# Optimization experiments

Hardware: AMD Instinct MI355X
Metric: run time of the kernel (lower is better)

## Reference

```python
import jax, jax.numpy as jnp
import numpy as np

B, S, HID = 1, 2048, 4096
NH, NKV, D = 32, 8, 128          # query heads, kv heads, head_dim
GROUPS = NH // NKV               # GQA repeat factor = 4
WINDOW = 1024                    # sliding-window size
ROPE_BASE = 10000.0


def setup_inputs() -> dict:
    key = jax.random.key(0)
    k = jax.random.split(key, 5)
    hidden_states = jax.random.normal(k[0], (B, S, HID), jnp.float32)
    Wq = jax.random.normal(k[1], (HID, HID), jnp.float32) * 0.02
    Wk = jax.random.normal(k[2], (NKV * D, HID), jnp.float32) * 0.02
    Wv = jax.random.normal(k[3], (NKV * D, HID), jnp.float32) * 0.02
    Wo = jax.random.normal(k[4], (HID, HID), jnp.float32) * 0.02
    position_ids = jnp.arange(S, dtype=jnp.int64 if jax.config.jax_enable_x64 else jnp.int32)[None, :]
    # Sliding-window causal additive mask [B,1,S,S]: key j visible to query i iff i-WINDOW < j <= i
    i = jnp.arange(S)
    visible = (i[None, :] <= i[:, None]) & (i[:, None] - i[None, :] < WINDOW)
    neg = jnp.finfo(jnp.float32).min
    attention_mask = jnp.where(visible, 0.0, neg)[None, None, :, :].astype(jnp.float32)
    return {"hidden_states": hidden_states, "attention_mask": attention_mask,
            "position_ids": position_ids, "Wq": Wq, "Wk": Wk, "Wv": Wv, "Wo": Wo}


def _rotate_half(x):
    x1, x2 = x[..., : D // 2], x[..., D // 2:]
    return jnp.concatenate((-x2, x1), axis=-1)


def _rope_cos_sin(position_ids, dtype):
    # inv_freq over even dims; gather-by-position_ids == direct indexing
    inv_freq = 1.0 / (ROPE_BASE ** (jnp.arange(0, D, 2, dtype=jnp.float32) / D))  # [D/2]
    freqs = position_ids.astype(jnp.float32)[..., None] * inv_freq                # [B,S,D/2]
    emb = jnp.concatenate((freqs, freqs), axis=-1)                                # [B,S,D]
    cos = jnp.cos(emb)[:, None, :, :].astype(dtype)                               # [B,1,S,D]
    sin = jnp.sin(emb)[:, None, :, :].astype(dtype)
    return cos, sin


def reference(hidden_states, attention_mask, position_ids, Wq, Wk, Wv, Wo):
    bsz, q_len, _ = hidden_states.shape
    # projections (nn.Linear: y = x @ W.T)
    q = (hidden_states @ Wq.T).reshape(bsz, q_len, NH, D).transpose(0, 2, 1, 3)    # [B,NH,S,D]
    k = (hidden_states @ Wk.T).reshape(bsz, q_len, NKV, D).transpose(0, 2, 1, 3)   # [B,NKV,S,D]
    v = (hidden_states @ Wv.T).reshape(bsz, q_len, NKV, D).transpose(0, 2, 1, 3)
    cos, sin = _rope_cos_sin(position_ids, q.dtype)
    q = q * cos + _rotate_half(q) * sin
    k = k * cos + _rotate_half(k) * sin
    # GQA repeat_kv (repeat_interleave along head dim)
    k = jnp.repeat(k, GROUPS, axis=1)                                              # [B,NH,S,D]
    v = jnp.repeat(v, GROUPS, axis=1)
    scores = jnp.einsum('bhqd,bhkd->bhqk', q, k) / np.sqrt(D)                       # [B,NH,S,S]
    scores = scores + attention_mask
    scores = jnp.maximum(scores, jnp.finfo(scores.dtype).min)
    probs = jax.nn.softmax(scores.astype(jnp.float32), axis=-1).astype(q.dtype)
    out = jnp.einsum('bhqk,bhkd->bhqd', probs, v)                                   # [B,NH,S,D]
    out = out.transpose(0, 2, 1, 3).reshape(bsz, q_len, HID)
    return out @ Wo.T
```

## Files before the change

### kernel.cpp

```cpp
#include <hip/hip_runtime.h>

#define S_LEN 2048
#define HID   4096
#define NH    32
#define NKV   8
#define DH    128
#define KVD   (NKV*DH)
#define WIN   1024
#define NTOT  6144

typedef __bf16 bf16_t;
typedef __bf16 bfrag  __attribute__((ext_vector_type(8)));
typedef __bf16 bf4    __attribute__((ext_vector_type(4)));
typedef float  ffrag  __attribute__((ext_vector_type(4)));
typedef float  f4     __attribute__((ext_vector_type(4)));

__global__ __launch_bounds__(256) void f32_to_bf16_kernel(const float* __restrict__ src,
                                                          bf16_t* __restrict__ dst, int n4) {
  int i = blockIdx.x * 256 + threadIdx.x;
  if (i < n4) {
    ffrag v = *(const ffrag*)(src + (size_t)i * 4);
    bf4 o;
    o[0] = (bf16_t)v[0]; o[1] = (bf16_t)v[1]; o[2] = (bf16_t)v[2]; o[3] = (bf16_t)v[3];
    *(bf4*)(dst + (size_t)i * 4) = o;
  }
}

__global__ __launch_bounds__(256) void cvt4_kernel(const float* __restrict__ h,
    const float* __restrict__ Wq, const float* __restrict__ Wk, const float* __restrict__ Wv,
    bf16_t* __restrict__ hB, bf16_t* __restrict__ WqB,
    bf16_t* __restrict__ WkB, bf16_t* __restrict__ WvB) {
  int i = blockIdx.x * 256 + threadIdx.x;
  const int N0 = S_LEN * HID / 4;
  const int N1 = N0 + HID * HID / 4;
  const int N2 = N1 + KVD * HID / 4;
  const float* s; bf16_t* d; int off;
  if (i < N0)      { s = h;  d = hB;  off = i; }
  else if (i < N1) { s = Wq; d = WqB; off = i - N0; }
  else if (i < N2) { s = Wk; d = WkB; off = i - N1; }
  else             { s = Wv; d = WvB; off = i - N2; }
  ffrag v = *(const ffrag*)(s + (size_t)off * 4);
  bf4 o;
  o[0] = (bf16_t)v[0]; o[1] = (bf16_t)v[1]; o[2] = (bf16_t)v[2]; o[3] = (bf16_t)v[3];
  *(bf4*)(d + (size_t)off * 4) = o;
}


__device__ __forceinline__ void load_lds16(const bf16_t* g, bf16_t* l) {
  __builtin_amdgcn_global_load_lds((__attribute__((address_space(1))) void*)g,
                                   (__attribute__((address_space(3))) void*)l,
                                   16, 0, 0);
}

#define BARW() asm volatile("s_barrier" ::: "memory")
#define WAITV(n) asm volatile("s_waitcnt vmcnt(" #n ")" ::: "memory")
#define LGKM0() do { asm volatile("s_waitcnt lgkmcnt(0)" ::: "memory"); \
                     __builtin_amdgcn_sched_barrier(0); } while (0)

template <int OUT_MODE>
__device__ __forceinline__ void gemm_body(const bf16_t* __restrict__ A,
                                          const bf16_t* __restrict__ B,
                                          void* __restrict__ Cv,
                                          int row0, int col0,
                                          int N, bf16_t* lds) {
  constexpr int K     = 4096;
  constexpr int NT    = K / 64;
  constexpr int ABUFE = 256 * 64;
  constexpr int BBUFE = 64 * 64;

  bf16_t* As0 = lds;
  bf16_t* Bs0 = lds + 2 * ABUFE;

  const int tid  = threadIdx.x;
  const int wave = tid >> 6;
  const int lane = tid & 63;
  const int wr = wave >> 2, wc = wave & 3;
  const int n = lane & 15, qd = lane >> 4;

  const int rsub = tid >> 3;
  const int sg   = (tid & 7) ^ (rsub & 7);
  const bf16_t* Ag = A + (size_t)(row0 + rsub) * K + sg * 8;
  const bf16_t* Bg = B + (size_t)(col0 + rsub) * K + sg * 8;
  const int wbase = wave * 512;

  const int pg0 = ( qd      ^ (n & 7)) * 8;
  const int pg1 = ((4 | qd) ^ (n & 7)) * 8;
  const int abase = wr * 8192 + n * 64;
  const int bbase = wc * 1024 + n * 64;

  ffrag acc[8];
#pragma unroll
  for (int mt = 0; mt < 8; ++mt) {
    acc[mt][0] = 0.f; acc[mt][1] = 0.f; acc[mt][2] = 0.f; acc[mt][3] = 0.f;
  }

  auto STAGE = [&](int t, int s) {
    const int ko = t * 64;
    bf16_t* as = As0 + s * ABUFE + wbase;
#pragma unroll
    for (int i = 0; i < 4; ++i)
      load_lds16(Ag + (size_t)(i * 64) * K + ko, as + i * 4096);
    load_lds16(Bg + ko, Bs0 + s * BBUFE + wbase);
  };

  STAGE(0, 0); STAGE(1, 1);
  WAITV(5);
  BARW();

  for (int t = 0; t < NT; ++t) {
    const int s = t & 1;
    const bf16_t* Asl = As0 + s * ABUFE;
    const bf16_t* Bsl = Bs0 + s * BBUFE;
    bfrag av[8], bv;

#pragma unroll
    for (int mt = 0; mt < 8; ++mt) av[mt] = *(const bfrag*)(Asl + abase + mt * 1024 + pg0);
    bv = *(const bfrag*)(Bsl + bbase + pg0);
    __builtin_amdgcn_s_setprio(1);
#pragma unroll
    for (int mt = 0; mt < 8; ++mt)
      acc[mt] = __builtin_amdgcn_mfma_f32_16x16x32_bf16(av[mt], bv, acc[mt], 0, 0, 0);
    __builtin_amdgcn_s_setprio(0);

#pragma unroll
    for (int mt = 0; mt < 8; ++mt) av[mt] = *(const bfrag*)(Asl + abase + mt * 1024 + pg1);
    bv = *(const bfrag*)(Bsl + bbase + pg1);
    __builtin_amdgcn_s_setprio(1);
#pragma unroll
    for (int mt = 0; mt < 8; ++mt)
      acc[mt] = __builtin_amdgcn_mfma_f32_16x16x32_bf16(av[mt], bv, acc[mt], 0, 0, 0);
    __builtin_amdgcn_s_setprio(0);

    LGKM0();
    BARW();
    if (t + 2 < NT) STAGE(t + 2, s);
    if (t + 1 < NT) {
      if (t + 2 < NT) { WAITV(5); }
      else            { WAITV(0); }
      BARW();
    }
  }

  const int orow = row0 + wr * 128 + qd * 4;
  const int ocol = col0 + wc * 16 + n;
#pragma unroll
  for (int mt = 0; mt < 8; ++mt)
#pragma unroll
    for (int r = 0; r < 4; ++r) {
      size_t idx = (size_t)(orow + mt * 16 + r) * N + ocol;
      if (OUT_MODE == 1) ((bf16_t*)Cv)[idx] = (bf16_t)acc[mt][r];
      else               ((float*)Cv)[idx]  = acc[mt][r];
    }
}

__global__ __launch_bounds__(512, 4) void gemm_qkv_kernel(const bf16_t* __restrict__ hB,
                                                          const bf16_t* __restrict__ Wqkv,
                                                          bf16_t* __restrict__ C) {
  __shared__ __align__(16) bf16_t lds[2 * 256 * 64 + 2 * 64 * 64];
  const int raw  = blockIdx.x;
  const int xcd  = raw & 7;
  const int slot = raw >> 3;
  const int bx   = xcd * 12 + slot % 12;
  const int by   = slot / 12;
  gemm_body<1>(hB, Wqkv, C, by * 256, bx * 64, NTOT, lds);
}

__global__ __launch_bounds__(512, 4) void gemm_out_kernel(const bf16_t* __restrict__ A,
                                                          const bf16_t* __restrict__ B,
                                                          float* __restrict__ out) {
  __shared__ __align__(16) bf16_t lds[2 * 256 * 64 + 2 * 64 * 64];
  const int raw  = blockIdx.x;
  const int xcd  = raw & 7;
  const int slot = raw >> 3;
  const int bx   = xcd * 8 + (slot & 7);
  const int by   = slot >> 3;
  gemm_body<0>(A, B, out, by * 256, bx * 64, HID, lds);
}

__global__ __launch_bounds__(256) void ropecvt_kernel(const bf16_t* __restrict__ Cqkv,
                                                      bf16_t* __restrict__ Qb,
                                                      bf16_t* __restrict__ Kb,
                                                      bf16_t* __restrict__ Vb) {
  int idx = blockIdx.x * 256 + threadIdx.x;
  int g  = idx & 7;
  int t  = idx >> 3;
  int hh = t % 48;
  int s  = t / 48;
  const bf16_t* r0 = Cqkv + (size_t)s * NTOT + hh * 128;
  bfrag a0 = *(const bfrag*)&r0[g * 8];
  bfrag a1 = *(const bfrag*)&r0[g * 8 + 64];
  bf16_t* p;
  bool rope;
  if (hh < NH)           { p = Qb + (size_t)s * HID + hh * DH;        rope = true; }
  else if (hh < NH+NKV)  { p = Kb + (size_t)s * KVD + (hh - NH) * DH; rope = true; }
  else                   { p = Vb + (size_t)s * KVD + (hh - 40) * DH; rope = false; }
  bfrag o1, o2;
#pragma unroll
  for (int j = 0; j < 8; ++j) {
    float x1 = (float)a0[j];
    float x2 = (float)a1[j];
    if (rope) {
      int d = g * 8 + j;
      float inv = exp2f((float)d * (-13.287712379549449f / 64.f));
      float ang = (float)s * inv;
      float sn = sinf(ang), cs = cosf(ang);
      o1[j] = (bf16_t)(x1 * cs - x2 * sn);
      o2[j] = (bf16_t)(x2 * cs + x1 * sn);
    } else {
      o1[j] = (bf16_t)x1;
      o2[j] = (bf16_t)x2;
    }
  }
  *(bfrag*)&p[g * 8]      = o1;
  *(bfrag*)&p[g * 8 + 64] = o2;
}

#define KS_STRIDE 136
#define VT_STRIDE 72
#define PS_STRIDE 72

__global__ __launch_bounds__(256, 3) void attn_kernel(const bf16_t* __restrict__ Q,
                                                      const bf16_t* __restrict__ Kc,
                                                      const bf16_t* __restrict__ Vc,
                                                      bf16_t* __restrict__ AO) {
  const int qt   = 31 - blockIdx.x;
  const int h    = blockIdx.y;
  const int kvh  = h >> 2;
  const int q0   = qt * 64;
  const int tid  = threadIdx.x;
  const int wq   = tid >> 6;
  const int lane = tid & 63;
  const int n    = lane & 15;
  const int quad = lane >> 4;
  const float scale = 0.08838834764831845f;

  __shared__ __align__(16) bf16_t Ks[64 * KS_STRIDE];
  __shared__ __align__(16) bf16_t VT[128 * VT_STRIDE];
  __shared__ __align__(16) bf16_t Ps[4][16 * PS_STRIDE];

  bfrag aq[4];
#pragma unroll
  for (int kc = 0; kc < 4; ++kc) {
    bfrag t = *(const bfrag*)&Q[(size_t)(q0 + wq * 16 + n) * HID + h * DH + kc * 32 + quad * 8];
#pragma unroll
    for (int e = 0; e < 8; ++e) t[e] = (bf16_t)((float)t[e] * scale);
    aq[kc] = t;
  }

  ffrag acc[8];
#pragma unroll
  for (int dt = 0; dt < 8; ++dt) { acc[dt][0] = 0.f; acc[dt][1] = 0.f; acc[dt][2] = 0.f; acc[dt][3] = 0.f; }
  float lrow[4] = {0.f, 0.f, 0.f, 0.f};

  const int ktlo = (q0 >= WIN) ? ((q0 - (WIN - 1)) >> 6) : 0;
  const int kthi = (q0 + 63) >> 6;

  const int kg = tid & 15;
  const int dg = tid >> 4;

  bfrag pk[4], pv[4];
  {
    const int k0 = ktlo * 64;
#pragma unroll
    for (int i = 0; i < 4; ++i) {
      int pos = i * 256 + tid;
      pk[i] = *(const bfrag*)&Kc[(size_t)(k0 + (pos >> 4)) * KVD + kvh * DH + (pos & 15) * 8];
    }
#pragma unroll
    for (int j = 0; j < 4; ++j)
      pv[j] = *(const bfrag*)&Vc[(size_t)(k0 + j * 16 + kg) * KVD + kvh * DH + dg * 8];
  }

  for (int kt = ktlo; kt <= kthi; ++kt) {
    const int k0 = kt * 64;
    __syncthreads();
#pragma unroll
    for (int i = 0; i < 4; ++i) {
      int pos = i * 256 + tid;
      *(bfrag*)&Ks[(pos >> 4) * KS_STRIDE + (pos & 15) * 8] = pk[i];
    }
#pragma unroll
    for (int i = 0; i < 8; ++i) {
      bf4 pkk;
      pkk[0] = pv[0][i]; pkk[1] = pv[1][i]; pkk[2] = pv[2][i]; pkk[3] = pv[3][i];
      *(bf4*)&VT[(dg * 8 + i) * VT_STRIDE + kg * 4] = pkk;
    }
    __syncthreads();
    if (kt < kthi) {
      const int k1 = k0 + 64;
#pragma unroll
      for (int i = 0; i < 4; ++i) {
        int pos = i * 256 + tid;
        pk[i] = *(const bfrag*)&Kc[(size_t)(k1 + (pos >> 4)) * KVD + kvh * DH + (pos & 15) * 8];
      }
#pragma unroll
      for (int j = 0; j < 4; ++j)
        pv[j] = *(const bfrag*)&Vc[(size_t)(k1 + j * 16 + kg) * KVD + kvh * DH + dg * 8];
    }

    ffrag s[4];
#pragma unroll
    for (int nt = 0; nt < 4; ++nt) { s[nt][0] = 0.f; s[nt][1] = 0.f; s[nt][2] = 0.f; s[nt][3] = 0.f; }
#pragma unroll
    for (int kc = 0; kc < 4; ++kc) {
      bfrag bk[4];
#pragma unroll
      for (int nt = 0; nt < 4; ++nt)
        bk[nt] = *(const bfrag*)&Ks[(nt * 16 + n) * KS_STRIDE + kc * 32 + quad * 8];
      __builtin_amdgcn_s_setprio(1);
#pragma unroll
      for (int nt = 0; nt < 4; ++nt)
        s[nt] = __builtin_amdgcn_mfma_f32_16x16x32_bf16(aq[kc], bk[nt], s[nt], 0, 0, 0);
      __builtin_amdgcn_s_setprio(0);
    }

    const bool full = (k0 + 63 <= q0) && (q0 + 63 - k0 < WIN);
    if (!full) {
#pragma unroll
      for (int nt = 0; nt < 4; ++nt)
#pragma unroll
        for (int r = 0; r < 4; ++r) {
          int q = q0 + wq * 16 + quad * 4 + r;
          int k = k0 + nt * 16 + n;
          bool vis = (k <= q) && ((q - k) < WIN);
          if (!vis) s[nt][r] = -1e30f;
        }
    }

#pragma unroll
    for (int r = 0; r < 4; ++r) {
      bf4 pkk;
      float ps0 = __expf(s[0][r]);
      float ps1 = __expf(s[1][r]);
      float ps2 = __expf(s[2][r]);
      float ps3 = __expf(s[3][r]);
      lrow[r] += (ps0 + ps1) + (ps2 + ps3);
      pkk[0] = (bf16_t)ps0; pkk[1] = (bf16_t)ps1; pkk[2] = (bf16_t)ps2; pkk[3] = (bf16_t)ps3;
      *(bf4*)&Ps[wq][(quad * 4 + r) * PS_STRIDE + n * 4] = pkk;
    }

#pragma unroll
    for (int kc = 0; kc < 2; ++kc) {
      bfrag ap = *(const bfrag*)&Ps[wq][n * PS_STRIDE + kc * 32 + quad * 8];
#pragma unroll
      for (int dt = 0; dt < 8; dt += 4) {
        bfrag bv0 = *(const bfrag*)&VT[((dt + 0) * 16 + n) * VT_STRIDE + kc * 32 + quad * 8];
        bfrag bv1 = *(const bfrag*)&VT[((dt + 1) * 16 + n) * VT_STRIDE + kc * 32 + quad * 8];
        bfrag bv2 = *(const bfrag*)&VT[((dt + 2) * 16 + n) * VT_STRIDE + kc * 32 + quad * 8];
        bfrag bv3 = *(const bfrag*)&VT[((dt + 3) * 16 + n) * VT_STRIDE + kc * 32 + quad * 8];
        __builtin_amdgcn_s_setprio(1);
        acc[dt + 0] = __builtin_amdgcn_mfma_f32_16x16x32_bf16(ap, bv0, acc[dt + 0], 0, 0, 0);
        acc[dt + 1] = __builtin_amdgcn_mfma_f32_16x16x32_bf16(ap, bv1, acc[dt + 1], 0, 0, 0);
        acc[dt + 2] = __builtin_amdgcn_mfma_f32_16x16x32_bf16(ap, bv2, acc[dt + 2], 0, 0, 0);
        acc[dt + 3] = __builtin_amdgcn_mfma_f32_16x16x32_bf16(ap, bv3, acc[dt + 3], 0, 0, 0);
        __builtin_amdgcn_s_setprio(0);
      }
    }
  }

#pragma unroll
  for (int off = 1; off < 16; off <<= 1)
#pragma unroll
    for (int r = 0; r < 4; ++r) lrow[r] += __shfl_xor(lrow[r], off);
  float inv[4];
#pragma unroll
  for (int r = 0; r < 4; ++r) inv[r] = 1.f / lrow[r];
#pragma unroll
  for (int dt = 0; dt < 8; ++dt)
#pragma unroll
    for (int r = 0; r < 4; ++r)
      AO[(size_t)(q0 + wq * 16 + quad * 4 + r) * HID + h * DH + dt * 16 + n] =
          (bf16_t)(acc[dt][r] * inv[r]);
}

extern "C" void kernel_launch(void* const* d_in, const int* in_sizes, int n_in,
                              void* d_out, int out_size, void* d_ws, size_t ws_size,
                              hipStream_t stream) {
  const float* h  = (const float*)d_in[0];
  const float* Wq = (const float*)d_in[3];
  const float* Wk = (const float*)d_in[4];
  const float* Wv = (const float*)d_in[5];
  const float* Wo = (const float*)d_in[6];
  float* out = (float*)d_out;

  char* ws = (char*)d_ws;
  const size_t MB = (size_t)1 << 20;
  bf16_t* hB    = (bf16_t*)(ws + 0 * MB);
  bf16_t* Qb    = (bf16_t*)(ws + 0 * MB);
  bf16_t* WqB   = (bf16_t*)(ws + 16 * MB);
  bf16_t* WkB   = (bf16_t*)(ws + 48 * MB);
  bf16_t* WvB   = (bf16_t*)(ws + 56 * MB);
  bf16_t* Cqkv  = (bf16_t*)(ws + 64 * MB);
  bf16_t* WoB   = (bf16_t*)(ws + 64 * MB);
  bf16_t* AOb   = (bf16_t*)(ws + 96 * MB);
  bf16_t* Kb    = (bf16_t*)(ws + 112 * MB);
  bf16_t* Vb    = (bf16_t*)(ws + 116 * MB);

  cvt4_kernel<<<(S_LEN * HID + HID * HID + 2 * KVD * HID) / 4 / 256, 256, 0, stream>>>(
      h, Wq, Wk, Wv, hB, WqB, WkB, WvB);

  gemm_qkv_kernel<<<768, 512, 0, stream>>>(hB, WqB, Cqkv);

  ropecvt_kernel<<<(S_LEN * 48 * 8) / 256, 256, 0, stream>>>(Cqkv, Qb, Kb, Vb);

  f32_to_bf16_kernel<<<(HID * HID / 4 + 255) / 256, 256, 0, stream>>>(Wo, WoB, HID * HID / 4);

  attn_kernel<<<dim3(32, NH), 256, 0, stream>>>(Qb, Kb, Vb, AOb);

  gemm_out_kernel<<<512, 512, 0, stream>>>(AOb, WoB, out);
}
```

Measured before the change: 464.7 us.

## Retile projection GEMMs to 128xBN blocks using 32x32x16 MFMA

Restructures both projection GEMMs from 256x64 tiles with 8 waves and 16x16x32 MFMAs to 128x192 (QKV) and 128x128 (output) tiles with 4 waves and 32x32x16 MFMAs. Each wave now computes a 64xWCOL sub-tile with 2xNB accumulators, which raises arithmetic intensity per LDS fragment load and balances A/B reuse better than the narrow 64-column tile. The trade-offs are more accumulator registers per wave, fewer waves per block, and a 512-block grid for the QKV GEMM where it used to be 768.

```diff
diff --git a/kernel.cpp b/kernel.cpp
--- a/kernel.cpp
+++ b/kernel.cpp
@@ -13,7 +13,7 @@
 typedef __bf16 bfrag  __attribute__((ext_vector_type(8)));
 typedef __bf16 bf4    __attribute__((ext_vector_type(4)));
 typedef float  ffrag  __attribute__((ext_vector_type(4)));
-typedef float  f4     __attribute__((ext_vector_type(4)));
+typedef float  facc   __attribute__((ext_vector_type(16)));
 
 __global__ __launch_bounds__(256) void f32_to_bf16_kernel(const float* __restrict__ src,
                                                           bf16_t* __restrict__ dst, int n4) {
@@ -57,7 +57,7 @@
 #define LGKM0() do { asm volatile("s_waitcnt lgkmcnt(0)" ::: "memory"); \
                      __builtin_amdgcn_sched_barrier(0); } while (0)
 
-template <int OUT_MODE>
+template <int BN, int OUT_MODE>
 __device__ __forceinline__ void gemm_body(const bf16_t* __restrict__ A,
                                           const bf16_t* __restrict__ B,
                                           void* __restrict__ Cv,
@@ -65,8 +65,11 @@
                                           int N, bf16_t* lds) {
   constexpr int K     = 4096;
   constexpr int NT    = K / 64;
-  constexpr int ABUFE = 256 * 64;
-  constexpr int BBUFE = 64 * 64;
+  constexpr int NB    = BN / 64;
+  constexpr int WCOL  = BN / 2;
+  constexpr int BSW   = BN / 32;
+  constexpr int ABUFE = 128 * 64;
+  constexpr int BBUFE = BN * 64;
 
   bf16_t* As0 = lds;
   bf16_t* Bs0 = lds + 2 * ABUFE;
@@ -74,8 +77,8 @@
   const int tid  = threadIdx.x;
   const int wave = tid >> 6;
   const int lane = tid & 63;
-  const int wr = wave >> 2, wc = wave & 3;
-  const int n = lane & 15, qd = lane >> 4;
+  const int wm = wave >> 1, wn = wave & 1;
+  const int l31 = lane & 31, hi = lane >> 5, l7 = lane & 7;
 
   const int rsub = tid >> 3;
   const int sg   = (tid & 7) ^ (rsub & 7);
@@ -83,98 +86,106 @@
   const bf16_t* Bg = B + (size_t)(col0 + rsub) * K + sg * 8;
   const int wbase = wave * 512;
 
-  const int pg0 = ( qd      ^ (n & 7)) * 8;
-  const int pg1 = ((4 | qd) ^ (n & 7)) * 8;
-  const int abase = wr * 8192 + n * 64;
-  const int bbase = wc * 1024 + n * 64;
-
-  ffrag acc[8];
-#pragma unroll
-  for (int mt = 0; mt < 8; ++mt) {
-    acc[mt][0] = 0.f; acc[mt][1] = 0.f; acc[mt][2] = 0.f; acc[mt][3] = 0.f;
-  }
+  int pgk[4];
+#pragma unroll
+  for (int ks = 0; ks < 4; ++ks) pgk[ks] = ((ks * 2 + hi) ^ l7) * 8;
+  const int aoff = (wm * 64 + l31) * 64;
+  const int boff = (wn * WCOL + l31) * 64;
+
+  facc acc[2][NB];
+#pragma unroll
+  for (int mt = 0; mt < 2; ++mt)
+#pragma unroll
+    for (int nt = 0; nt < NB; ++nt)
+#pragma unroll
+      for (int j = 0; j < 16; ++j) acc[mt][nt][j] = 0.f;
 
   auto STAGE = [&](int t, int s) {
     const int ko = t * 64;
     bf16_t* as = As0 + s * ABUFE + wbase;
+    bf16_t* bs = Bs0 + s * BBUFE + wbase;
 #pragma unroll
     for (int i = 0; i < 4; ++i)
-      load_lds16(Ag + (size_t)(i * 64) * K + ko, as + i * 4096);
-    load_lds16(Bg + ko, Bs0 + s * BBUFE + wbase);
+      load_lds16(Ag + (size_t)(i * 32) * K + ko, as + i * 2048);
+#pragma unroll
+    for (int i = 0; i < BSW; ++i)
+      load_lds16(Bg + (size_t)(i * 32) * K + ko, bs + i * 2048);
   };
 
   STAGE(0, 0); STAGE(1, 1);
-  WAITV(5);
+  if constexpr (BN == 192) { WAITV(10); } else { WAITV(8); }
   BARW();
 
   for (int t = 0; t < NT; ++t) {
     const int s = t & 1;
     const bf16_t* Asl = As0 + s * ABUFE;
     const bf16_t* Bsl = Bs0 + s * BBUFE;
-    bfrag av[8], bv;
-
-#pragma unroll
-    for (int mt = 0; mt < 8; ++mt) av[mt] = *(const bfrag*)(Asl + abase + mt * 1024 + pg0);
-    bv = *(const bfrag*)(Bsl + bbase + pg0);
-    __builtin_amdgcn_s_setprio(1);
-#pragma unroll
-    for (int mt = 0; mt < 8; ++mt)
-      acc[mt] = __builtin_amdgcn_mfma_f32_16x16x32_bf16(av[mt], bv, acc[mt], 0, 0, 0);
-    __builtin_amdgcn_s_setprio(0);
-
-#pragma unroll
-    for (int mt = 0; mt < 8; ++mt) av[mt] = *(const bfrag*)(Asl + abase + mt * 1024 + pg1);
-    bv = *(const bfrag*)(Bsl + bbase + pg1);
-    __builtin_amdgcn_s_setprio(1);
-#pragma unroll
-    for (int mt = 0; mt < 8; ++mt)
-      acc[mt] = __builtin_amdgcn_mfma_f32_16x16x32_bf16(av[mt], bv, acc[mt], 0, 0, 0);
-    __builtin_amdgcn_s_setprio(0);
+
+#pragma unroll
+    for (int ks = 0; ks < 4; ++ks) {
+      bfrag av0 = *(const bfrag*)(Asl + aoff + pgk[ks]);
+      bfrag av1 = *(const bfrag*)(Asl + aoff + 2048 + pgk[ks]);
+      bfrag bv[NB];
+#pragma unroll
+      for (int nt = 0; nt < NB; ++nt)
+        bv[nt] = *(const bfrag*)(Bsl + boff + nt * 2048 + pgk[ks]);
+      __builtin_amdgcn_s_setprio(1);
+#pragma unroll
+      for (int nt = 0; nt < NB; ++nt)
+        acc[0][nt] = __builtin_amdgcn_mfma_f32_32x32x16_bf16(av0, bv[nt], acc[0][nt], 0, 0, 0);
+#pragma unroll
+      for (int nt = 0; nt < NB; ++nt)
+        acc[1][nt] = __builtin_amdgcn_mfma_f32_32x32x16_bf16(av1, bv[nt], acc[1][nt], 0, 0, 0);
+      __builtin_amdgcn_s_setprio(0);
+    }
 
     LGKM0();
     BARW();
     if (t + 2 < NT) STAGE(t + 2, s);
     if (t + 1 < NT) {
-      if (t + 2 < NT) { WAITV(5); }
+      if (t + 2 < NT) { if constexpr (BN == 192) { WAITV(10); } else { WAITV(8); } }
       else            { WAITV(0); }
       BARW();
     }
   }
 
-  const int orow = row0 + wr * 128 + qd * 4;
-  const int ocol = col0 + wc * 16 + n;
-#pragma unroll
-  for (int mt = 0; mt < 8; ++mt)
-#pragma unroll
-    for (int r = 0; r < 4; ++r) {
-      size_t idx = (size_t)(orow + mt * 16 + r) * N + ocol;
-      if (OUT_MODE == 1) ((bf16_t*)Cv)[idx] = (bf16_t)acc[mt][r];
-      else               ((float*)Cv)[idx]  = acc[mt][r];
-    }
-}
-
-__global__ __launch_bounds__(512, 4) void gemm_qkv_kernel(const bf16_t* __restrict__ hB,
+  const int orow = row0 + wm * 64 + 4 * hi;
+  const int ocol = col0 + wn * WCOL + l31;
+#pragma unroll
+  for (int mt = 0; mt < 2; ++mt)
+#pragma unroll
+    for (int nt = 0; nt < NB; ++nt)
+#pragma unroll
+      for (int j = 0; j < 16; ++j) {
+        int r = orow + mt * 32 + (j & 3) + 8 * (j >> 2);
+        size_t idx = (size_t)r * N + (ocol + nt * 32);
+        if (OUT_MODE == 1) ((bf16_t*)Cv)[idx] = (bf16_t)acc[mt][nt][j];
+        else               ((float*)Cv)[idx]  = acc[mt][nt][j];
+      }
+}
+
+__global__ __launch_bounds__(256, 2) void gemm_qkv_kernel(const bf16_t* __restrict__ hB,
                                                           const bf16_t* __restrict__ Wqkv,
                                                           bf16_t* __restrict__ C) {
-  __shared__ __align__(16) bf16_t lds[2 * 256 * 64 + 2 * 64 * 64];
+  __shared__ __align__(16) bf16_t lds[2 * 128 * 64 + 2 * 192 * 64];
   const int raw  = blockIdx.x;
   const int xcd  = raw & 7;
   const int slot = raw >> 3;
-  const int bx   = xcd * 12 + slot % 12;
-  const int by   = slot / 12;
-  gemm_body<1>(hB, Wqkv, C, by * 256, bx * 64, NTOT, lds);
-}
-
-__global__ __launch_bounds__(512, 4) void gemm_out_kernel(const bf16_t* __restrict__ A,
+  const int bx   = xcd * 4 + (slot & 3);
+  const int by   = slot >> 2;
+  gemm_body<192, 1>(hB, Wqkv, C, by * 128, bx * 192, NTOT, lds);
+}
+
+__global__ __launch_bounds__(256, 2) void gemm_out_kernel(const bf16_t* __restrict__ A,
                                                           const bf16_t* __restrict__ B,
                                                           float* __restrict__ out) {
-  __shared__ __align__(16) bf16_t lds[2 * 256 * 64 + 2 * 64 * 64];
+  __shared__ __align__(16) bf16_t lds[2 * 128 * 64 + 2 * 128 * 64];
   const int raw  = blockIdx.x;
   const int xcd  = raw & 7;
   const int slot = raw >> 3;
-  const int bx   = xcd * 8 + (slot & 7);
-  const int by   = slot >> 3;
-  gemm_body<0>(A, B, out, by * 256, bx * 64, HID, lds);
+  const int bx   = xcd * 4 + (slot & 3);
+  const int by   = slot >> 2;
+  gemm_body<128, 0>(A, B, out, by * 128, bx * 128, HID, lds);
 }
 
 __global__ __launch_bounds__(256) void ropecvt_kernel(const bf16_t* __restrict__ Cqkv,
@@ -399,7 +410,7 @@
   cvt4_kernel<<<(S_LEN * HID + HID * HID + 2 * KVD * HID) / 4 / 256, 256, 0, stream>>>(
       h, Wq, Wk, Wv, hB, WqB, WkB, WvB);
 
-  gemm_qkv_kernel<<<768, 512, 0, stream>>>(hB, WqB, Cqkv);
+  gemm_qkv_kernel<<<512, 256, 0, stream>>>(hB, WqB, Cqkv);
 
   ropecvt_kernel<<<(S_LEN * 48 * 8) / 256, 256, 0, stream>>>(Cqkv, Qb, Kb, Vb);
 
@@ -407,5 +418,5 @@
 
   attn_kernel<<<dim3(32, NH), 256, 0, stream>>>(Qb, Kb, Vb, AOb);
 
-  gemm_out_kernel<<<512, 512, 0, stream>>>(AOb, WoB, out);
-}
+  gemm_out_kernel<<<512, 256, 0, stream>>>(AOb, WoB, out);
+}
```

After: 458.5 us. About the same (-1.3%).
